# Performance work log

Hardware: AMD Instinct MI355X
Metric: run time of the kernel (lower is better)

## Reference

```python
import jax, jax.numpy as jnp
import numpy as np

TEMPERATURE = 22.627417  # ~sqrt(512)


def setup_inputs() -> dict:
    key = jax.random.key(0)
    ks = jax.random.split(key, 7)
    B, NP, NQ, D = 4, 256, 256, 512
    return {
        "q": jax.random.normal(ks[0], (B, NP, D), jnp.float32),
        "k": jax.random.normal(ks[1], (B, NP, D), jnp.float32),
        "v": jax.random.normal(ks[2], (B, NP, D), jnp.float32),
        "query": jax.random.normal(ks[3], (B, NQ, D), jnp.float32),
        "query_q": jax.random.normal(ks[4], (B, NQ, D), jnp.float32),
        "query_k": jax.random.normal(ks[5], (B, NP, D), jnp.float32),
        "query_v": jax.random.normal(ks[6], (B, NQ, D), jnp.float32),
    }


def reference(q, k, v, query, query_q, query_k, query_v):
    # Self-attention block over prototypes: [B, NP, NP]
    scores = jnp.einsum("bpd,bqd->bpq", q, k) / TEMPERATURE
    log_attn = jax.nn.log_softmax(scores, axis=2)
    attn = jax.nn.softmax(scores, axis=2)
    # NOTE: torch.bmm(attn, v) in the original is dead code (overwritten), so it is skipped.

    # Query-gated attention: [B, NQ, NP]
    q_scores = jnp.einsum("bnd,bpd->bnp", query_q, query_k) / TEMPERATURE
    query_attn = jax.nn.softmax(q_scores, axis=2)

    # Gated broadcast combine: [B, NQ, NP, D]
    # query_attn * v_rep + query_attn * query_v == query_attn * (v + query_v)
    gate = query_attn[:, :, :, None]            # [B, NQ, NP, 1]
    combined = v[:, None, :, :] + query_v[:, :, None, :]  # [B, NQ, NP, D]
    output = gate * combined
    return (output, attn, log_attn)
```

## Files before the change

kernel.cpp:

```cpp
#include <hip/hip_runtime.h>
#include <math.h>

#define BB   4
#define NP   256
#define NQ   256
#define DD   512
#define DD4  (DD / 4)

typedef float f32x4 __attribute__((ext_vector_type(4)));

static constexpr float kScale = 1.0f / 22.627417f;

__global__ __launch_bounds__(256) void fused_qgsa2_kernel(
    const float* __restrict__ q,
    const float* __restrict__ k,
    const f32x4* __restrict__ v4,
    const float* __restrict__ qq,
    const float* __restrict__ qk,
    const f32x4* __restrict__ qv4,
    f32x4* __restrict__ out4,
    float* __restrict__ attn_out,
    float* __restrict__ logattn_out)
{
    __shared__ __align__(16) float smem[4 * 256];
    const int t = threadIdx.x;

    if (blockIdx.x < 512u) {
        const int b  = blockIdx.x >> 7;
        const int n0 = (blockIdx.x & 127) * 2;

        {
            const f32x4* krow = (const f32x4*)(qk + ((size_t)b * NP + t) * DD);
            const float* qb   = qq + ((size_t)b * NQ + n0) * DD;
            float acc0 = 0.f, acc1 = 0.f;
            #pragma unroll 8
            for (int d4 = 0; d4 < DD4; ++d4) {
                const f32x4 kv = krow[d4];
                const float* q0 = qb + d4 * 4;
                const float* q1 = qb + DD + d4 * 4;
                acc0 += q0[0] * kv.x + q0[1] * kv.y + q0[2] * kv.z + q0[3] * kv.w;
                acc1 += q1[0] * kv.x + q1[1] * kv.y + q1[2] * kv.z + q1[3] * kv.w;
            }
            smem[t]       = acc0 * kScale;
            smem[256 + t] = acc1 * kScale;
        }
        __syncthreads();

        {
            const int r = (t >> 6) & 1;
            const int g = t & 63;
            const f32x4 sv = ((const f32x4*)(smem + r * 256))[g];

            float m = fmaxf(fmaxf(sv.x, sv.y), fmaxf(sv.z, sv.w));
            #pragma unroll
            for (int off = 32; off >= 1; off >>= 1)
                m = fmaxf(m, __shfl_xor(m, off, 64));

            f32x4 ev;
            ev.x = expf(sv.x - m); ev.y = expf(sv.y - m);
            ev.z = expf(sv.z - m); ev.w = expf(sv.w - m);
            float s = (ev.x + ev.y) + (ev.z + ev.w);
            #pragma unroll
            for (int off = 32; off >= 1; off >>= 1) s += __shfl_xor(s, off, 64);

            const float inv = 1.0f / s;
            float* gtf = smem + 512;
            gtf[(4 * g + 0) * 2 + r] = ev.x * inv;
            gtf[(4 * g + 1) * 2 + r] = ev.y * inv;
            gtf[(4 * g + 2) * 2 + r] = ev.z * inv;
            gtf[(4 * g + 3) * 2 + r] = ev.w * inv;
        }
        __syncthreads();

        const int d4 = t & (DD4 - 1);
        const int po = t >> 7;
        const f32x4 qvr0 = qv4[((size_t)b * NQ + n0) * DD4 + d4];
        const f32x4 qvr1 = qv4[((size_t)b * NQ + n0 + 1) * DD4 + d4];
        const f32x4* vcol = v4 + (size_t)b * NP * DD4 + d4;
        f32x4* ocol = out4 + ((size_t)b * NQ + n0) * ((size_t)NP * DD4) + d4;
        const float2* gt2 = (const float2*)(smem + 512);

        #pragma unroll 4
        for (int p = po; p < NP; p += 2) {
            const f32x4 vv = vcol[(size_t)p * DD4];
            const float2 g2 = gt2[p];
            __builtin_nontemporal_store((vv + qvr0) * g2.x,
                                        ocol + (size_t)p * DD4);
            __builtin_nontemporal_store((vv + qvr1) * g2.y,
                                        ocol + (size_t)(NP * DD4) + (size_t)p * DD4);
        }
    } else {
        const int idx = blockIdx.x - 512;
        const int b   = idx >> 6;
        const int p0  = (idx & 63) * 4;

        const f32x4* krow = (const f32x4*)(k + ((size_t)b * NP + t) * DD);
        const float* qb   = q + ((size_t)b * NP + p0) * DD;

        float acc[4] = {0.f, 0.f, 0.f, 0.f};
        #pragma unroll 8
        for (int d4 = 0; d4 < DD4; ++d4) {
            const f32x4 kv = krow[d4];
            #pragma unroll
            for (int r = 0; r < 4; ++r) {
                const float* qr = qb + r * DD + d4 * 4;
                acc[r] += qr[0] * kv.x + qr[1] * kv.y + qr[2] * kv.z + qr[3] * kv.w;
            }
        }

        float (*ss)[256] = (float (*)[256])smem;
        #pragma unroll
        for (int r = 0; r < 4; ++r) ss[r][t] = acc[r] * kScale;
        __syncthreads();

        const int r = t >> 6;
        const int g = t & 63;
        const f32x4 sv = ((const f32x4*)ss[r])[g];

        float m = fmaxf(fmaxf(sv.x, sv.y), fmaxf(sv.z, sv.w));
        #pragma unroll
        for (int off = 32; off >= 1; off >>= 1)
            m = fmaxf(m, __shfl_xor(m, off, 64));

        f32x4 ev;
        ev.x = expf(sv.x - m); ev.y = expf(sv.y - m);
        ev.z = expf(sv.z - m); ev.w = expf(sv.w - m);
        float s = (ev.x + ev.y) + (ev.z + ev.w);
        #pragma unroll
        for (int off = 32; off >= 1; off >>= 1) s += __shfl_xor(s, off, 64);

        const float inv = 1.0f / s;
        const float lse = logf(s);

        const size_t base = ((size_t)b * NP + (p0 + r)) * 256;
        ((f32x4*)(attn_out + base))[g] = ev * inv;
        f32x4 lg;
        lg.x = (sv.x - m) - lse; lg.y = (sv.y - m) - lse;
        lg.z = (sv.z - m) - lse; lg.w = (sv.w - m) - lse;
        ((f32x4*)(logattn_out + base))[g] = lg;
    }
}

extern "C" void kernel_launch(void* const* d_in, const int* in_sizes, int n_in,
                              void* d_out, int out_size, void* d_ws, size_t ws_size,
                              hipStream_t stream) {
    const float* q  = (const float*)d_in[0];
    const float* k  = (const float*)d_in[1];
    const float* v  = (const float*)d_in[2];
    const float* qq = (const float*)d_in[4];
    const float* qk = (const float*)d_in[5];
    const float* qv = (const float*)d_in[6];

    float* out = (float*)d_out;
    const size_t out_elems = (size_t)BB * NQ * NP * DD;
    float* attn_out    = out + out_elems;
    float* logattn_out = attn_out + (size_t)BB * NP * 256;

    fused_qgsa2_kernel<<<768, 256, 0, stream>>>(
        q, k, (const f32x4*)v, qq, qk, (const f32x4*)qv,
        (f32x4*)out, attn_out, logattn_out);
}
```

Before: 137.5 us.

## Split gate softmax into separate kernel and tile store over 8 queries x 32 prototypes

The query-gate softmax moves into its own kernel, which computes four rows per block. It writes the gate values into the first floats of each output tile, using the output buffer as scratch. The store kernel then reads its own tile's 256 gate values, keeps 8 query_v rows in registers, and writes an 8x32 (query, prototype) tile. This drops the per-block QK recomputation from the store path and cuts repeated v reads, since each v row is reused across 8 queries instead of 2. The cost is an extra kernel launch and a dependence between the two kernels through the scratch slots in the output buffer.

Result: slower. 145.9 us (+6.1%).

```diff
diff --git a/kernel.cpp b/kernel.cpp
--- a/kernel.cpp
+++ b/kernel.cpp
@@ -11,86 +11,107 @@
 
 static constexpr float kScale = 1.0f / 22.627417f;
 
-__global__ __launch_bounds__(256) void fused_qgsa2_kernel(
+__global__ __launch_bounds__(256) void gate_kernel(
+    const float* __restrict__ qq,
+    const float* __restrict__ qk,
+    float* __restrict__ outf)
+{
+    const int b  = blockIdx.y;
+    const int n0 = blockIdx.x * 4;
+    const int t  = threadIdx.x;
+
+    const f32x4* krow = (const f32x4*)(qk + ((size_t)b * NP + t) * DD);
+    const float* qb   = qq + ((size_t)b * NQ + n0) * DD;
+
+    float acc[4] = {0.f, 0.f, 0.f, 0.f};
+    #pragma unroll 8
+    for (int d4 = 0; d4 < DD4; ++d4) {
+        const f32x4 kv = krow[d4];
+        #pragma unroll
+        for (int r = 0; r < 4; ++r) {
+            const float* qr = qb + r * DD + d4 * 4;
+            acc[r] += qr[0] * kv.x + qr[1] * kv.y + qr[2] * kv.z + qr[3] * kv.w;
+        }
+    }
+
+    __shared__ __align__(16) float ss[4][256];
+    #pragma unroll
+    for (int r = 0; r < 4; ++r) ss[r][t] = acc[r] * kScale;
+    __syncthreads();
+
+    const int r = t >> 6;
+    const int g = t & 63;
+    const f32x4 sv = ((const f32x4*)ss[r])[g];
+
+    float m = fmaxf(fmaxf(sv.x, sv.y), fmaxf(sv.z, sv.w));
+    #pragma unroll
+    for (int off = 32; off >= 1; off >>= 1) m = fmaxf(m, __shfl_xor(m, off, 64));
+
+    f32x4 ev;
+    ev.x = expf(sv.x - m); ev.y = expf(sv.y - m);
+    ev.z = expf(sv.z - m); ev.w = expf(sv.w - m);
+    float s = (ev.x + ev.y) + (ev.z + ev.w);
+    #pragma unroll
+    for (int off = 32; off >= 1; off >>= 1) s += __shfl_xor(s, off, 64);
+    const float inv = 1.0f / s;
+
+    const int n  = n0 + r;
+    const int ng = n >> 3, nr = n & 7;
+    const int c0 = 4 * g;
+    const int pr = c0 >> 5;
+    float* slot = outf
+        + (((size_t)(b * NQ + (ng << 3))) * NP + (pr << 5)) * DD
+        + nr * 32 + (c0 & 31);
+    *(f32x4*)slot = ev * inv;
+}
+
+__global__ __launch_bounds__(256) void store_kernel(
     const float* __restrict__ q,
     const float* __restrict__ k,
     const f32x4* __restrict__ v4,
-    const float* __restrict__ qq,
-    const float* __restrict__ qk,
     const f32x4* __restrict__ qv4,
-    f32x4* __restrict__ out4,
+    float* __restrict__ outf,
     float* __restrict__ attn_out,
     float* __restrict__ logattn_out)
 {
     __shared__ __align__(16) float smem[4 * 256];
     const int t = threadIdx.x;
 
-    if (blockIdx.x < 512u) {
-        const int b  = blockIdx.x >> 7;
-        const int n0 = (blockIdx.x & 127) * 2;
+    if (blockIdx.x < 1024u) {
+        const int idx  = blockIdx.x;
+        const int b    = idx >> 8;
+        const int rest = idx & 255;
+        const int n0   = (rest >> 3) << 3;
+        const int p0   = (rest & 7) << 5;
 
-        {
-            const f32x4* krow = (const f32x4*)(qk + ((size_t)b * NP + t) * DD);
-            const float* qb   = qq + ((size_t)b * NQ + n0) * DD;
-            float acc0 = 0.f, acc1 = 0.f;
-            #pragma unroll 8
-            for (int d4 = 0; d4 < DD4; ++d4) {
-                const f32x4 kv = krow[d4];
-                const float* q0 = qb + d4 * 4;
-                const float* q1 = qb + DD + d4 * 4;
-                acc0 += q0[0] * kv.x + q0[1] * kv.y + q0[2] * kv.z + q0[3] * kv.w;
-                acc1 += q1[0] * kv.x + q1[1] * kv.y + q1[2] * kv.z + q1[3] * kv.w;
-            }
-            smem[t]       = acc0 * kScale;
-            smem[256 + t] = acc1 * kScale;
-        }
-        __syncthreads();
-
-        {
-            const int r = (t >> 6) & 1;
-            const int g = t & 63;
-            const f32x4 sv = ((const f32x4*)(smem + r * 256))[g];
-
-            float m = fmaxf(fmaxf(sv.x, sv.y), fmaxf(sv.z, sv.w));
-            #pragma unroll
-            for (int off = 32; off >= 1; off >>= 1)
-                m = fmaxf(m, __shfl_xor(m, off, 64));
-
-            f32x4 ev;
-            ev.x = expf(sv.x - m); ev.y = expf(sv.y - m);
-            ev.z = expf(sv.z - m); ev.w = expf(sv.w - m);
-            float s = (ev.x + ev.y) + (ev.z + ev.w);
-            #pragma unroll
-            for (int off = 32; off >= 1; off >>= 1) s += __shfl_xor(s, off, 64);
-
-            const float inv = 1.0f / s;
-            float* gtf = smem + 512;
-            gtf[(4 * g + 0) * 2 + r] = ev.x * inv;
-            gtf[(4 * g + 1) * 2 + r] = ev.y * inv;
-            gtf[(4 * g + 2) * 2 + r] = ev.z * inv;
-            gtf[(4 * g + 3) * 2 + r] = ev.w * inv;
-        }
+        const float* slot = outf + (((size_t)(b * NQ + n0)) * NP + p0) * DD;
+        smem[t] = slot[t];
         __syncthreads();
 
         const int d4 = t & (DD4 - 1);
         const int po = t >> 7;
-        const f32x4 qvr0 = qv4[((size_t)b * NQ + n0) * DD4 + d4];
-        const f32x4 qvr1 = qv4[((size_t)b * NQ + n0 + 1) * DD4 + d4];
-        const f32x4* vcol = v4 + (size_t)b * NP * DD4 + d4;
-        f32x4* ocol = out4 + ((size_t)b * NQ + n0) * ((size_t)NP * DD4) + d4;
-        const float2* gt2 = (const float2*)(smem + 512);
+        const f32x4* qvb = qv4 + ((size_t)(b * NQ + n0)) * DD4 + d4;
+        f32x4 qvr[8];
+        #pragma unroll
+        for (int r = 0; r < 8; ++r) qvr[r] = qvb[(size_t)r * DD4];
 
-        #pragma unroll 4
-        for (int p = po; p < NP; p += 2) {
+        const f32x4* vcol  = v4 + ((size_t)b * NP) * DD4 + d4;
+        f32x4*       obase = (f32x4*)outf + (((size_t)(b * NQ + n0)) * NP) * DD4 + d4;
+
+        #pragma unroll 2
+        for (int pi = 0; pi < 16; ++pi) {
+            const int p  = p0 + 2 * pi + po;
+            const int pc = 2 * pi + po;
             const f32x4 vv = vcol[(size_t)p * DD4];
-            const float2 g2 = gt2[p];
-            __builtin_nontemporal_store((vv + qvr0) * g2.x,
-                                        ocol + (size_t)p * DD4);
-            __builtin_nontemporal_store((vv + qvr1) * g2.y,
-                                        ocol + (size_t)(NP * DD4) + (size_t)p * DD4);
+            #pragma unroll
+            for (int r = 0; r < 8; ++r) {
+                const float gpn = smem[r * 32 + pc];
+                __builtin_nontemporal_store((vv + qvr[r]) * gpn,
+                    obase + ((size_t)r * NP + p) * DD4);
+            }
         }
     } else {
-        const int idx = blockIdx.x - 512;
+        const int idx = blockIdx.x - 1024;
         const int b   = idx >> 6;
         const int p0  = (idx & 63) * 4;
 
@@ -156,7 +177,8 @@
     float* attn_out    = out + out_elems;
     float* logattn_out = attn_out + (size_t)BB * NP * 256;
 
-    fused_qgsa2_kernel<<<768, 256, 0, stream>>>(
-        q, k, (const f32x4*)v, qq, qk, (const f32x4*)qv,
-        (f32x4*)out, attn_out, logattn_out);
+    gate_kernel<<<dim3(NQ / 4, BB), 256, 0, stream>>>(qq, qk, out);
+
+    store_kernel<<<1280, 256, 0, stream>>>(
+        q, k, (const f32x4*)v, (const f32x4*)qv, out, attn_out, logattn_out);
 }
```
